# Performance work log

Measured on AMD Instinct MI355X. Metric: run time of the kernel, lower is better.

The kernel has to match this reference:

```python
import jax, jax.numpy as jnp
from jax import lax
import numpy as np

VOCAB, EMB, HID, ENC, ATT, P = 10000, 512, 1024, 2048, 512, 196
B, T = 64, 160
PAD_IDX = 3

def setup_inputs() -> dict:
    key = jax.random.key(0)
    ks = jax.random.split(key, 20)
    s = 0.02
    emb = jax.random.normal(ks[0], (VOCAB, EMB), jnp.float32) * s
    emb = emb.at[PAD_IDX].set(0.0)
    return {
        'image_embedding': jax.random.normal(ks[1], (B, P, ENC), jnp.float32),
        'padded_sentence': jax.random.randint(ks[2], (B, T), 0, VOCAB),
        'enc_h': jax.random.normal(ks[3], (2, B, HID // 2), jnp.float32),
        'enc_c': jax.random.normal(ks[4], (2, B, HID // 2), jnp.float32),
        'sentence_lens': jax.random.randint(ks[5], (B,), 1, T + 1),
        'emb': emb,
        'Wea': jax.random.normal(ks[6], (ATT, ENC), jnp.float32) * s,
        'bea': jnp.zeros((ATT,), jnp.float32),
        'Wda': jax.random.normal(ks[7], (ATT, HID), jnp.float32) * s,
        'bda': jnp.zeros((ATT,), jnp.float32),
        'wfa': jax.random.normal(ks[8], (ATT,), jnp.float32) * s,
        'bfa': jnp.zeros((), jnp.float32),
        'Wfb': jax.random.normal(ks[9], (ENC, HID), jnp.float32) * s,
        'bfb': jnp.zeros((ENC,), jnp.float32),
        'Wih': jax.random.normal(ks[10], (4 * HID, EMB + ENC), jnp.float32) * s,
        'bih': jnp.zeros((4 * HID,), jnp.float32),
        'Whh': jax.random.normal(ks[11], (4 * HID, HID), jnp.float32) * s,
        'bhh': jnp.zeros((4 * HID,), jnp.float32),
    }


def reference(image_embedding, padded_sentence, enc_h, enc_c, sentence_lens,
              emb, Wea, bea, Wda, bda, wfa, bfa, Wfb, bfb, Wih, bih, Whh, bhh):
    Tn = padded_sentence.shape[1]
    # sort by descending length (replicates sentence_lens.sort(descending=True))
    idx = jnp.argsort(-sentence_lens)
    img = image_embedding[idx]                   # [B,P,E]
    sent = padded_sentence[idx]                  # [B,T]
    lens = sentence_lens[idx]                    # [B]
    h0 = jnp.concatenate([enc_h[-2], enc_h[-1]], axis=1)[idx]  # [B,HID]
    c0 = jnp.concatenate([enc_c[-2], enc_c[-1]], axis=1)[idx]
    emb_eff = emb.at[PAD_IDX].set(0.0)           # padding_idx=3
    x_emb = emb_eff[sent]                        # [B,T,EMB]
    # encoder projection is h-independent: hoist out of the scan
    att1 = jnp.einsum('bpe,ae->bpa', img, Wea) + bea  # [B,P,ATT]

    def step(carry, xt):
        h, c = carry
        x_t, t = xt
        active = (t < lens)[:, None]             # ragged mask
        att2 = h @ Wda.T + bda                   # [B,ATT]
        e = jax.nn.relu(att1 + att2[:, None, :]) @ wfa + bfa  # [B,P]
        alpha = jax.nn.softmax(e, axis=1)
        context = jnp.einsum('bp,bpe->be', alpha, img)        # [B,ENC]
        gate = jax.nn.sigmoid(h @ Wfb.T + bfb)
        inp = jnp.concatenate([x_t, gate * context], axis=1)  # [B,EMB+ENC]
        gates = inp @ Wih.T + bih + h @ Whh.T + bhh           # [B,4*HID]
        i, f, g, o = jnp.split(gates, 4, axis=1)
        c_new = jax.nn.sigmoid(f) * c + jax.nn.sigmoid(i) * jnp.tanh(g)
        h_new = jax.nn.sigmoid(o) * jnp.tanh(c_new)
        h = jnp.where(active, h_new, h)
        c = jnp.where(active, c_new, c)
        out_t = jnp.where(active, h_new, 0.0)
        alpha_t = jnp.where(active, alpha, 0.0)
        return (h, c), (out_t, alpha_t)

    (_, _), (outs, alphas) = lax.scan(
        step, (h0, c0), (jnp.swapaxes(x_emb, 0, 1), jnp.arange(Tn)))
    outputs = jnp.swapaxes(outs, 0, 1)           # [B,T,HID]
    alphas = jnp.swapaxes(alphas, 0, 1)          # [B,T,P]
    # replicate the original's final reindex (outputs[ordered_idx], not inverse)
    return outputs[idx], alphas[idx]
```

## Files before the change

kernel.cpp:

```cpp
#include <hip/hip_runtime.h>
#include <hip/hip_bf16.h>
#include <math.h>

#define B 64
#define T 160
#define P 196
#define ENC 2048
#define ATT 512
#define EMB 512
#define HID 1024
#define KTOT 3584
#define N2 2560
#define KT4 112
#define NTHR 1024
#define NBLK 256
#define NGRP 16
#define GRPSZ (NBLK/NGRP)

typedef __attribute__((ext_vector_type(8))) short bf16x8;
typedef __attribute__((ext_vector_type(4))) float f32x4;
typedef float __attribute__((ext_vector_type(4))) vf4;

__device__ __forceinline__ float sigm(float x){ return 1.0f/(1.0f+__expf(-x)); }
__device__ __forceinline__ float bfu(short s){ return __uint_as_float(((unsigned)(unsigned short)s) << 16); }

__device__ __forceinline__ float ldgf(const float* p){ return *(const volatile float*)p; }
__device__ __forceinline__ void stgf(float* p, float v){ *(volatile float*)p = v; }
__device__ __forceinline__ void stgu(unsigned* p, unsigned v){ *(volatile unsigned*)p = v; }
__device__ __forceinline__ unsigned pkbf(float a, float b){
    unsigned ua = (unsigned)__bfloat16_as_ushort(__float2bfloat16(a));
    unsigned ub = (unsigned)__bfloat16_as_ushort(__float2bfloat16(b));
    return ua | (ub << 16);
}

__device__ __forceinline__ void gbar(unsigned* bar, unsigned k){
    asm volatile("s_waitcnt vmcnt(0)" ::: "memory");
    __syncthreads();
    if (threadIdx.x == 0){
        unsigned g = blockIdx.x & (NGRP-1);
        unsigned* gcnt = bar + g*256;
        unsigned* top  = bar + NGRP*256;
        unsigned old = __hip_atomic_fetch_add(gcnt, 1u, __ATOMIC_RELAXED, __HIP_MEMORY_SCOPE_AGENT);
        if (old == (k + 1u)*GRPSZ - 1u){
            __hip_atomic_fetch_add(top, 1u, __ATOMIC_RELAXED, __HIP_MEMORY_SCOPE_AGENT);
        }
        unsigned target = (k + 1u)*NGRP;
        while (*(volatile unsigned*)top < target){
            __builtin_amdgcn_s_sleep(1);
        }
    }
    __syncthreads();
    asm volatile("" ::: "memory");
}

__global__ void k_sort(const int* lens, int* idx, int* rank, unsigned* barCnt, int* nAct){
    __shared__ int L[B];
    int i = threadIdx.x;
    L[i] = lens[i];
    if (i <= NGRP) barCnt[i*256] = 0u;
    __syncthreads();
    int li = L[i];
    int r = 0;
    for (int j = 0; j < B; ++j){
        int lj = L[j];
        if (lj > li || (lj == li && j < i)) r++;
    }
    rank[i] = r;
    idx[r] = i;
    for (int tt = i; tt < T; tt += B){
        int c = 0;
        for (int j = 0; j < B; ++j) c += (L[j] > tt) ? 1 : 0;
        nAct[tt] = c;
    }
}

__global__ void k_init_hc(const float* enc_h, const float* enc_c, const int* idx,
                          float* h, float* c, __hip_bfloat16* hbR0){
    int j = blockIdx.x;
    int o = idx[j];
    for (int k = threadIdx.x; k < HID; k += blockDim.x){
        float hv = (k < 512) ? enc_h[o*512 + k] : enc_h[B*512 + o*512 + (k-512)];
        float cv = (k < 512) ? enc_c[o*512 + k] : enc_c[B*512 + o*512 + (k-512)];
        h[j*HID + k] = hv;
        c[j*HID + k] = cv;
        hbR0[j*HID + k] = __float2bfloat16(hv);
    }
}

__global__ void k_cvt_wcat(const float* Wih, const float* Whh, __hip_bfloat16* Wfrag){
    size_t i = (size_t)blockIdx.x*256 + threadIdx.x;
    int e = (int)(i & 7);
    size_t t2 = i >> 3;
    int lane = (int)(t2 & 63);
    size_t t3 = t2 >> 6;
    int kt = (int)(t3 % KT4);
    int strip = (int)(t3 / KT4);
    int n = strip*16 + (lane & 15);
    int r = (n & 3)*HID + (n >> 2);
    int k = kt*32 + (lane >> 4)*8 + e;
    float v = (k < EMB+ENC) ? Wih[(size_t)r*(EMB+ENC) + k]
                            : Whh[(size_t)r*HID + (k - EMB - ENC)];
    Wfrag[i] = __float2bfloat16(v);
}

__global__ void k_bsum(const float* bih, const float* bhh, float* bsum){
    int n = blockIdx.x*256 + threadIdx.x;
    int r = (n & 3)*HID + (n >> 2);
    bsum[n] = bih[r] + bhh[r];
}

__global__ void k_cvt_w2(const float* Wda, const float* bda, const float* Wfb, const float* bfb,
                         __hip_bfloat16* W2, float* bias2){
    int n = blockIdx.x;
    const float* src = (n < ATT) ? (Wda + (size_t)n*HID) : (Wfb + (size_t)(n-ATT)*HID);
    __hip_bfloat16* dst = W2 + (size_t)n*HID;
    for (int k = threadIdx.x; k < HID; k += 256) dst[k] = __float2bfloat16(src[k]);
    if (threadIdx.x == 0) bias2[n] = (n < ATT) ? bda[n] : bfb[n-ATT];
}

__global__ void k_cvt_emb(const float* emb, __hip_bfloat16* emb_bf){
    size_t i = (size_t)blockIdx.x*256 + threadIdx.x;
    emb_bf[i] = __float2bfloat16(emb[i]);
}

__global__ void k_cvt_wea(const float* Wea, __hip_bfloat16* Wea_bf){
    int n = blockIdx.x;
    for (int k = threadIdx.x; k < ENC; k += 256)
        Wea_bf[(size_t)n*ENC + k] = __float2bfloat16(Wea[(size_t)n*ENC + k]);
}

__global__ void k_cvt_img(const float* img, const int* idx, __hip_bfloat16* img_s){
    int j = blockIdx.y;
    int o = idx[j];
    size_t off = (size_t)blockIdx.x*256 + threadIdx.x;
    img_s[(size_t)j*P*ENC + off] = __float2bfloat16(img[(size_t)o*P*ENC + off]);
}

__global__ __launch_bounds__(256) void k_att1m(const __hip_bfloat16* img_s, const __hip_bfloat16* Wea_bf,
                                               const float* bea, __hip_bfloat16* att1w){
    int m0 = blockIdx.x * 64, n0 = blockIdx.y * 64;
    int tid = threadIdx.x, w = tid >> 6, l = tid & 63, lm = l & 15, lk = l >> 4;
    const short* ap = (const short*)img_s + (size_t)(m0 + 16*w + lm)*ENC + 8*lk;
    const short* bp = (const short*)Wea_bf + (size_t)(n0 + lm)*ENC + 8*lk;
    f32x4 acc[4];
    #pragma unroll
    for (int nt=0; nt<4; ++nt) acc[nt] = (f32x4){0.f,0.f,0.f,0.f};
    #pragma unroll 4
    for (int kt = 0; kt < ENC/32; ++kt){
        bf16x8 a = *(const bf16x8*)(ap + kt*32);
        #pragma unroll
        for (int nt=0; nt<4; ++nt){
            bf16x8 bb = *(const bf16x8*)(bp + (size_t)nt*16*ENC + kt*32);
            acc[nt] = __builtin_amdgcn_mfma_f32_16x16x32_bf16(a, bb, acc[nt], 0,0,0);
        }
    }
    #pragma unroll
    for (int nt=0; nt<4; ++nt){
        int n = n0 + nt*16 + lm;
        float bv = bea[n];
        #pragma unroll
        for (int r=0; r<4; ++r){
            int m = m0 + 16*w + 4*lk + r;
            att1w[(size_t)m*ATT + n] = __float2bfloat16(acc[nt][r] + bv);
        }
    }
}

struct SP {
    const __hip_bfloat16 *att1w, *img_s, *emb_bf, *Wfrag, *W2;
    const float *bsum, *bias2, *wfa, *bfa;
    const int *sent, *idx, *rank, *lens, *nAct;
    float *D2;
    __hip_bfloat16 *gcR, *hbR;
    float *hF0, *hF1, *cW;
    float *outH, *outA;
    unsigned *barCnt;
};

__global__ __launch_bounds__(1024, 4) void k_scan(SP p){
    __shared__ short WcatL[KT4*64*8];
    __shared__ union {
        struct { float Dp[4][64][17]; float hS[64][4]; int tokL[64], lensL[64], wLs[64]; } gem;
        struct { float att2L[512]; float wfaL[512]; float red[1024]; float aL[208]; float ctxP[8][512]; } p23;
    } sh;

    int b = blockIdx.x, tid = threadIdx.x;
    int w = tid >> 6, l = tid & 63, lm = l & 15, lk = l >> 4;
    unsigned bk = 0;

    {
        const bf16x8* src = (const bf16x8*)((const short*)p.Wfrag + (size_t)b*KT4*64*8);
        bf16x8* dst = (bf16x8*)WcatL;
        #pragma unroll
        for (int i = 0; i < KT4*64/NTHR; ++i) dst[tid + i*NTHR] = src[tid + i*NTHR];
    }
    __syncthreads();

    float bfa0 = p.bfa[0];

    for (int t = 0; t < T; ++t){
        const __hip_bfloat16* hbIn = p.hbR + (size_t)t*B*HID;
        __hip_bfloat16*       hbOut = p.hbR + (size_t)(t+1)*B*HID;
        const __hip_bfloat16* gcT  = p.gcR + (size_t)t*B*ENC;
        const float* hFIn = (t & 1) ? p.hF1 : p.hF0;
        float*       hFOut = (t & 1) ? p.hF0 : p.hF1;
        int nAct = p.nAct[t];

        if (b < N2/16){
            int n0 = b*16;
            int rt = w & 3, kq = w >> 2;
            if (16*rt < nAct){
                const short* ap = (const short*)hbIn + (size_t)(16*rt + lm)*HID + kq*256 + 8*lk;
                const short* bp = (const short*)p.W2 + (size_t)(n0 + lm)*HID + kq*256 + 8*lk;
                f32x4 acc = {0.f,0.f,0.f,0.f};
                #pragma unroll
                for (int kt = 0; kt < 8; ++kt){
                    bf16x8 a = *(const bf16x8*)(ap + kt*32);
                    bf16x8 bb = *(const bf16x8*)(bp + kt*32);
                    acc = __builtin_amdgcn_mfma_f32_16x16x32_bf16(a, bb, acc, 0,0,0);
                }
                #pragma unroll
                for (int r=0; r<4; ++r) sh.gem.Dp[kq][16*rt + 4*lk + r][lm] = acc[r];
            }
            __syncthreads();
            int m = tid >> 4, nl = tid & 15;
            if (m < nAct){
                stgf(&p.D2[m*N2 + n0 + nl],
                     sh.gem.Dp[0][m][nl] + sh.gem.Dp[1][m][nl]
                   + sh.gem.Dp[2][m][nl] + sh.gem.Dp[3][m][nl] + p.bias2[n0 + nl]);
            }
        }
        gbar(p.barCnt, bk++);

        {
            int j = b & 63, q = b >> 6;
            int o = p.idx[j], wj = p.rank[j], lj = p.lens[o];
            if (t < lj){
                if (tid < 512){
                    sh.p23.att2L[tid] = ldgf(&p.D2[j*N2 + tid]);
                    sh.p23.wfaL[tid]  = p.wfa[tid];
                }
                __syncthreads();

                int pp = tid & 255, ah = tid >> 8;
                float acc = 0.f;
                if (pp < P){
                    const short* ar = (const short*)p.att1w + (size_t)(j*P + pp)*ATT + ah*128;
                    #pragma unroll 8
                    for (int k8 = 0; k8 < 16; ++k8){
                        bf16x8 v = *(const bf16x8*)(ar + k8*8);
                        #pragma unroll
                        for (int z=0; z<8; ++z){
                            int a = ah*128 + k8*8 + z;
                            acc += fmaxf(bfu(v[z]) + sh.p23.att2L[a], 0.f) * sh.p23.wfaL[a];
                        }
                    }
                }
                sh.p23.red[tid] = acc;
                __syncthreads();
                float e = -1e30f;
                if (tid < P) e = sh.p23.red[tid] + sh.p23.red[tid+256] + sh.p23.red[tid+512] + sh.p23.red[tid+768] + bfa0;
                __syncthreads();
                sh.p23.red[tid] = (tid < P) ? e : -1e30f;
                __syncthreads();
                for (int s = 512; s > 0; s >>= 1){
                    if (tid < s) sh.p23.red[tid] = fmaxf(sh.p23.red[tid], sh.p23.red[tid+s]);
                    __syncthreads();
                }
                float m = sh.p23.red[0];
                __syncthreads();
                float ex = (tid < P) ? __expf(e - m) : 0.f;
                sh.p23.red[tid] = ex;
                __syncthreads();
                for (int s = 512; s > 0; s >>= 1){
                    if (tid < s) sh.p23.red[tid] += sh.p23.red[tid+s];
                    __syncthreads();
                }
                float ssum = sh.p23.red[0];
                if (tid < P){
                    float alpha = ex / ssum;
                    sh.p23.aL[tid] = alpha;
                    if (q == 0) p.outA[((size_t)(wj*T + t))*P + tid] = alpha;
                }
                if (tid >= P && tid < 208) sh.p23.aL[tid] = 0.f;
                __syncthreads();

                const short* ib = (const short*)p.img_s + (size_t)j*P*ENC + q*512 + l*8;
                float a8[8];
                #pragma unroll
                for (int z=0; z<8; ++z) a8[z] = 0.f;
                #pragma unroll 4
                for (int i = 0; i < 13; ++i){
                    int pp2 = w + 16*i;
                    int pr = (pp2 < P) ? pp2 : 0;
                    bf16x8 v = *(const bf16x8*)(ib + (size_t)pr*ENC);
                    float al = sh.p23.aL[pp2];
                    #pragma unroll
                    for (int z=0; z<8; ++z) a8[z] += al * bfu(v[z]);
                }
                if (w < 8){
                    #pragma unroll
                    for (int z=0; z<8; ++z) sh.p23.ctxP[w][l*8+z] = a8[z];
                }
                __syncthreads();
                if (w >= 8){
                    #pragma unroll
                    for (int z=0; z<8; ++z) sh.p23.ctxP[w-8][l*8+z] += a8[z];
                }
                __syncthreads();
                if (tid < 256){
                    int d0 = 2*tid;
                    float c0 = 0.f, c1 = 0.f;
                    #pragma unroll
                    for (int r=0; r<8; ++r){ c0 += sh.p23.ctxP[r][d0]; c1 += sh.p23.ctxP[r][d0+1]; }
                    int eg0 = q*512 + d0;
                    float g0 = sigm(ldgf(&p.D2[j*N2 + ATT + eg0]));
                    float g1 = sigm(ldgf(&p.D2[j*N2 + ATT + eg0 + 1]));
                    stgu((unsigned*)((short*)gcT + j*ENC + eg0), pkbf(g0*c0, g1*c1));
                }
            } else {
                if (q == 0 && tid < P) p.outA[((size_t)(wj*T + t))*P + tid] = 0.f;
            }
        }
        gbar(p.barCnt, bk++);

        {
            if (tid < 64){
                int o = p.idx[tid];
                sh.gem.tokL[tid] = p.sent[o*T + t];
                sh.gem.lensL[tid] = p.lens[o];
                sh.gem.wLs[tid] = p.rank[tid];
            }
            __syncthreads();
            int rt = w & 3, kq = w >> 2;
            if (16*rt < nAct){
                int mrow = 16*rt + lm;
                int tok = sh.gem.tokL[mrow];
                const short* aEmb = (const short*)p.emb_bf + (size_t)tok*EMB + 8*lk;
                const short* aGc  = (const short*)gcT + (size_t)mrow*ENC + 8*lk;
                const short* aH   = (const short*)hbIn + (size_t)mrow*HID + 8*lk;
                const bf16x8* BL = (const bf16x8*)WcatL;
                f32x4 acc = {0.f,0.f,0.f,0.f};
                if (kq == 0){
                    #pragma unroll 8
                    for (int kt = 0; kt < 16; ++kt){
                        bf16x8 a = *(const bf16x8*)(aEmb + kt*32);
                        acc = __builtin_amdgcn_mfma_f32_16x16x32_bf16(a, BL[kt*64 + l], acc, 0,0,0);
                    }
                    #pragma unroll 6
                    for (int kt = 16; kt < 28; ++kt){
                        bf16x8 a = *(const bf16x8*)(aGc + (kt-16)*32);
                        acc = __builtin_amdgcn_mfma_f32_16x16x32_bf16(a, BL[kt*64 + l], acc, 0,0,0);
                    }
                } else if (kq == 1){
                    #pragma unroll 7
                    for (int kt = 28; kt < 56; ++kt){
                        bf16x8 a = *(const bf16x8*)(aGc + (kt-16)*32);
                        acc = __builtin_amdgcn_mfma_f32_16x16x32_bf16(a, BL[kt*64 + l], acc, 0,0,0);
                    }
                } else if (kq == 2){
                    #pragma unroll 6
                    for (int kt = 56; kt < 80; ++kt){
                        bf16x8 a = *(const bf16x8*)(aGc + (kt-16)*32);
                        acc = __builtin_amdgcn_mfma_f32_16x16x32_bf16(a, BL[kt*64 + l], acc, 0,0,0);
                    }
                    #pragma unroll
                    for (int kt = 80; kt < 84; ++kt){
                        bf16x8 a = *(const bf16x8*)(aH + (kt-80)*32);
                        acc = __builtin_amdgcn_mfma_f32_16x16x32_bf16(a, BL[kt*64 + l], acc, 0,0,0);
                    }
                } else {
                    #pragma unroll 7
                    for (int kt = 84; kt < 112; ++kt){
                        bf16x8 a = *(const bf16x8*)(aH + (kt-80)*32);
                        acc = __builtin_amdgcn_mfma_f32_16x16x32_bf16(a, BL[kt*64 + l], acc, 0,0,0);
                    }
                }
                #pragma unroll
                for (int r=0; r<4; ++r) sh.gem.Dp[kq][16*rt + 4*lk + r][lm] = acc[r];
            }
            __syncthreads();
            if (tid < 256){
                int j2 = tid & 63, du = tid >> 6;
                int u = 4*b + du;
                float g4[4];
                #pragma unroll
                for (int g=0; g<4; ++g){
                    int nl = 4*du + g;
                    g4[g] = sh.gem.Dp[0][j2][nl] + sh.gem.Dp[1][j2][nl]
                          + sh.gem.Dp[2][j2][nl] + sh.gem.Dp[3][j2][nl] + p.bsum[16*b + nl];
                }
                float ig = sigm(g4[0]), fg = sigm(g4[1]), gg = tanhf(g4[2]), og = sigm(g4[3]);
                float cOld = p.cW[j2*HID + u];
                float cNew = fg*cOld + ig*gg;
                float hNew = og*tanhf(cNew);
                bool active = (t < sh.gem.lensL[j2]);
                float hOld = hFIn[j2*HID + u];
                float hKeep = active ? hNew : hOld;
                hFOut[j2*HID + u] = hKeep;
                sh.gem.hS[j2][du] = hKeep;
                p.cW[j2*HID + u] = active ? cNew : cOld;
                p.outH[((size_t)sh.gem.wLs[j2]*T + t)*HID + u] = active ? hNew : 0.f;
            }
            __syncthreads();
            if (tid < 128){
                int j2 = tid & 63, dp = tid >> 6;
                int u0 = 4*b + 2*dp;
                stgu((unsigned*)((short*)hbOut + j2*HID + u0),
                     pkbf(sh.gem.hS[j2][2*dp], sh.gem.hS[j2][2*dp+1]));
            }
        }
        gbar(p.barCnt, bk++);
    }
}

extern "C" void kernel_launch(void* const* d_in, const int* in_sizes, int n_in,
                              void* d_out, int out_size, void* d_ws, size_t ws_size,
                              hipStream_t stream) {
    const float* img   = (const float*)d_in[0];
    const int*   sent  = (const int*)  d_in[1];
    const float* enc_h = (const float*)d_in[2];
    const float* enc_c = (const float*)d_in[3];
    const int*   lens  = (const int*)  d_in[4];
    const float* emb   = (const float*)d_in[5];
    const float* Wea   = (const float*)d_in[6];
    const float* bea   = (const float*)d_in[7];
    const float* Wda   = (const float*)d_in[8];
    const float* bda   = (const float*)d_in[9];
    const float* wfa   = (const float*)d_in[10];
    const float* bfa   = (const float*)d_in[11];
    const float* Wfb   = (const float*)d_in[12];
    const float* bfb   = (const float*)d_in[13];
    const float* Wih   = (const float*)d_in[14];
    const float* bih   = (const float*)d_in[15];
    const float* Whh   = (const float*)d_in[16];
    const float* bhh   = (const float*)d_in[17];

    float* outH = (float*)d_out;
    float* outA = outH + (size_t)B*T*HID;

    char* wsb = (char*)d_ws;
    size_t off = 0;
    int* idxW  = (int*)(wsb + off); off += 256;
    int* rankW = (int*)(wsb + off); off += 256;
    int* nActW = (int*)(wsb + off); off += 1024;
    unsigned* barCnt = (unsigned*)(wsb + off); off += 32768;
    __hip_bfloat16* att1w = (__hip_bfloat16*)(wsb + off); off += (size_t)B*P*ATT*2;
    __hip_bfloat16* img_s = (__hip_bfloat16*)(wsb + off); off += (size_t)B*P*ENC*2;
    __hip_bfloat16* emb_bf= (__hip_bfloat16*)(wsb + off); off += (size_t)10000*EMB*2;
    __hip_bfloat16* Wfrag = (__hip_bfloat16*)(wsb + off); off += (size_t)4*HID*KTOT*2;
    __hip_bfloat16* W2    = (__hip_bfloat16*)(wsb + off); off += (size_t)N2*HID*2;
    __hip_bfloat16* Wea_bf= (__hip_bfloat16*)(wsb + off); off += (size_t)ATT*ENC*2;
    float* bsum  = (float*)(wsb + off); off += 4*HID*4;
    float* bias2 = (float*)(wsb + off); off += N2*4;
    float* hA    = (float*)(wsb + off); off += B*HID*4;
    float* hB    = (float*)(wsb + off); off += B*HID*4;
    float* cWs   = (float*)(wsb + off); off += B*HID*4;
    float* D2    = (float*)(wsb + off); off += (size_t)B*N2*4;
    __hip_bfloat16* gcR = (__hip_bfloat16*)(wsb + off); off += (size_t)T*B*ENC*2;
    __hip_bfloat16* hbR = (__hip_bfloat16*)(wsb + off); off += (size_t)(T+1)*B*HID*2;

    k_sort<<<1, 64, 0, stream>>>(lens, idxW, rankW, barCnt, nActW);
    k_init_hc<<<B, 256, 0, stream>>>(enc_h, enc_c, idxW, hA, cWs, hbR);
    k_cvt_wcat<<<57344, 256, 0, stream>>>(Wih, Whh, Wfrag);
    k_bsum<<<16, 256, 0, stream>>>(bih, bhh, bsum);
    k_cvt_w2<<<N2, 256, 0, stream>>>(Wda, bda, Wfb, bfb, W2, bias2);
    k_cvt_emb<<<20000, 256, 0, stream>>>(emb, emb_bf);
    k_cvt_wea<<<ATT, 256, 0, stream>>>(Wea, Wea_bf);
    k_cvt_img<<<dim3(P*ENC/256, B), 256, 0, stream>>>(img, idxW, img_s);
    k_att1m<<<dim3((B*P)/64, ATT/64), 256, 0, stream>>>(img_s, Wea_bf, bea, att1w);

    SP sp;
    sp.att1w = att1w; sp.img_s = img_s; sp.emb_bf = emb_bf; sp.Wfrag = Wfrag; sp.W2 = W2;
    sp.bsum = bsum; sp.bias2 = bias2; sp.wfa = wfa; sp.bfa = bfa;
    sp.sent = sent; sp.idx = idxW; sp.rank = rankW; sp.lens = lens; sp.nAct = nActW;
    sp.D2 = D2; sp.gcR = gcR; sp.hbR = hbR;
    sp.hF0 = hA; sp.hF1 = hB; sp.cW = cWs;
    sp.outH = outH; sp.outA = outA;
    sp.barCnt = barCnt;

    void* args[] = { &sp };
    hipLaunchCooperativeKernel(reinterpret_cast<void*>(k_scan), dim3(NBLK), dim3(NTHR),
                               args, 0, stream);
}
```

Baseline: 7.452 ms.

## Split grid barrier into arrive/wait with hierarchical release and overlap work

```diff
diff --git a/kernel.cpp b/kernel.cpp
--- a/kernel.cpp
+++ b/kernel.cpp
@@ -33,31 +33,42 @@
     return ua | (ub << 16);
 }
 
-__device__ __forceinline__ void gbar(unsigned* bar, unsigned k){
+__device__ __forceinline__ void gbar_arrive(unsigned* bar, unsigned k){
     asm volatile("s_waitcnt vmcnt(0)" ::: "memory");
     __syncthreads();
     if (threadIdx.x == 0){
         unsigned g = blockIdx.x & (NGRP-1);
-        unsigned* gcnt = bar + g*256;
-        unsigned* top  = bar + NGRP*256;
-        unsigned old = __hip_atomic_fetch_add(gcnt, 1u, __ATOMIC_RELAXED, __HIP_MEMORY_SCOPE_AGENT);
+        unsigned old = __hip_atomic_fetch_add(bar + g*256, 1u, __ATOMIC_RELAXED, __HIP_MEMORY_SCOPE_AGENT);
         if (old == (k + 1u)*GRPSZ - 1u){
-            __hip_atomic_fetch_add(top, 1u, __ATOMIC_RELAXED, __HIP_MEMORY_SCOPE_AGENT);
-        }
-        unsigned target = (k + 1u)*NGRP;
-        while (*(volatile unsigned*)top < target){
-            __builtin_amdgcn_s_sleep(1);
+            __hip_atomic_fetch_add(bar + NGRP*256, 1u, __ATOMIC_RELAXED, __HIP_MEMORY_SCOPE_AGENT);
+        }
+    }
+}
+__device__ __forceinline__ void gbar_wait(unsigned* bar, unsigned k){
+    if (threadIdx.x == 0){
+        unsigned b = blockIdx.x;
+        if (b < NGRP){
+            volatile unsigned* top = bar + NGRP*256;
+            while (*top < (k + 1u)*NGRP) __builtin_amdgcn_s_sleep(2);
+            *(volatile unsigned*)(bar + (NGRP + 1 + b)*256) = k + 1u;
+        } else {
+            volatile unsigned* rel = bar + (NGRP + 1 + (b & (NGRP-1)))*256;
+            while (*rel < k + 1u) __builtin_amdgcn_s_sleep(2);
         }
     }
     __syncthreads();
     asm volatile("" ::: "memory");
+}
+__device__ __forceinline__ void gbar(unsigned* bar, unsigned k){
+    gbar_arrive(bar, k);
+    gbar_wait(bar, k);
 }
 
 __global__ void k_sort(const int* lens, int* idx, int* rank, unsigned* barCnt, int* nAct){
     __shared__ int L[B];
     int i = threadIdx.x;
     L[i] = lens[i];
-    if (i <= NGRP) barCnt[i*256] = 0u;
+    if (i < 33) barCnt[i*256] = 0u;
     __syncthreads();
     int li = L[i];
     int r = 0;
@@ -230,14 +241,14 @@
                    + sh.gem.Dp[2][m][nl] + sh.gem.Dp[3][m][nl] + p.bias2[n0 + nl]);
             }
         }
-        gbar(p.barCnt, bk++);
-
+        gbar(p.barCnt, bk); bk++;
+
+        int jj = b & 63, qq = b >> 6;
+        int oo = p.idx[jj], wjj = p.rank[jj], ljj = p.lens[oo];
         {
-            int j = b & 63, q = b >> 6;
-            int o = p.idx[j], wj = p.rank[j], lj = p.lens[o];
-            if (t < lj){
+            if (t < ljj){
                 if (tid < 512){
-                    sh.p23.att2L[tid] = ldgf(&p.D2[j*N2 + tid]);
+                    sh.p23.att2L[tid] = ldgf(&p.D2[jj*N2 + tid]);
                     sh.p23.wfaL[tid]  = p.wfa[tid];
                 }
                 __syncthreads();
@@ -245,7 +256,7 @@
                 int pp = tid & 255, ah = tid >> 8;
                 float acc = 0.f;
                 if (pp < P){
-                    const short* ar = (const short*)p.att1w + (size_t)(j*P + pp)*ATT + ah*128;
+                    const short* ar = (const short*)p.att1w + (size_t)(jj*P + pp)*ATT + ah*128;
                     #pragma unroll 8
                     for (int k8 = 0; k8 < 16; ++k8){
                         bf16x8 v = *(const bf16x8*)(ar + k8*8);
@@ -277,15 +288,11 @@
                     __syncthreads();
                 }
                 float ssum = sh.p23.red[0];
-                if (tid < P){
-                    float alpha = ex / ssum;
-                    sh.p23.aL[tid] = alpha;
-                    if (q == 0) p.outA[((size_t)(wj*T + t))*P + tid] = alpha;
-                }
+                if (tid < P) sh.p23.aL[tid] = ex / ssum;
                 if (tid >= P && tid < 208) sh.p23.aL[tid] = 0.f;
                 __syncthreads();
 
-                const short* ib = (const short*)p.img_s + (size_t)j*P*ENC + q*512 + l*8;
+                const short* ib = (const short*)p.img_s + (size_t)jj*P*ENC + qq*512 + l*8;
                 float a8[8];
                 #pragma unroll
                 for (int z=0; z<8; ++z) a8[z] = 0.f;
@@ -313,40 +320,64 @@
                     float c0 = 0.f, c1 = 0.f;
                     #pragma unroll
                     for (int r=0; r<8; ++r){ c0 += sh.p23.ctxP[r][d0]; c1 += sh.p23.ctxP[r][d0+1]; }
-                    int eg0 = q*512 + d0;
-                    float g0 = sigm(ldgf(&p.D2[j*N2 + ATT + eg0]));
-                    float g1 = sigm(ldgf(&p.D2[j*N2 + ATT + eg0 + 1]));
-                    stgu((unsigned*)((short*)gcT + j*ENC + eg0), pkbf(g0*c0, g1*c1));
-                }
-            } else {
-                if (q == 0 && tid < P) p.outA[((size_t)(wj*T + t))*P + tid] = 0.f;
+                    int eg0 = qq*512 + d0;
+                    float g0 = sigm(ldgf(&p.D2[jj*N2 + ATT + eg0]));
+                    float g1 = sigm(ldgf(&p.D2[jj*N2 + ATT + eg0 + 1]));
+                    stgu((unsigned*)((short*)gcT + jj*ENC + eg0), pkbf(g0*c0, g1*c1));
+                }
             }
         }
-        gbar(p.barCnt, bk++);
-
+        gbar_arrive(p.barCnt, bk);
+
+        if (qq == 0 && tid < P){
+            float av = (t < ljj) ? sh.p23.aL[tid] : 0.f;
+            p.outA[((size_t)(wjj*T + t))*P + tid] = av;
+        }
+        __syncthreads();
+
+        if (tid < 64){
+            int o = p.idx[tid];
+            sh.gem.tokL[tid] = p.sent[o*T + t];
+            sh.gem.lensL[tid] = p.lens[o];
+            sh.gem.wLs[tid] = p.rank[tid];
+        }
+        __syncthreads();
         {
-            if (tid < 64){
-                int o = p.idx[tid];
-                sh.gem.tokL[tid] = p.sent[o*T + t];
-                sh.gem.lensL[tid] = p.lens[o];
-                sh.gem.wLs[tid] = p.rank[tid];
-            }
-            __syncthreads();
             int rt = w & 3, kq = w >> 2;
-            if (16*rt < nAct){
-                int mrow = 16*rt + lm;
+            bool act = (16*rt < nAct);
+            int mrow = 16*rt + lm;
+            f32x4 acc = {0.f,0.f,0.f,0.f};
+            const short* aEmb = 0; const short* aGc = 0; const short* aH = 0;
+            const bf16x8* BL = (const bf16x8*)WcatL;
+            if (act){
                 int tok = sh.gem.tokL[mrow];
-                const short* aEmb = (const short*)p.emb_bf + (size_t)tok*EMB + 8*lk;
-                const short* aGc  = (const short*)gcT + (size_t)mrow*ENC + 8*lk;
-                const short* aH   = (const short*)hbIn + (size_t)mrow*HID + 8*lk;
-                const bf16x8* BL = (const bf16x8*)WcatL;
-                f32x4 acc = {0.f,0.f,0.f,0.f};
+                aEmb = (const short*)p.emb_bf + (size_t)tok*EMB + 8*lk;
+                aGc  = (const short*)gcT + (size_t)mrow*ENC + 8*lk;
+                aH   = (const short*)hbIn + (size_t)mrow*HID + 8*lk;
                 if (kq == 0){
                     #pragma unroll 8
                     for (int kt = 0; kt < 16; ++kt){
                         bf16x8 a = *(const bf16x8*)(aEmb + kt*32);
                         acc = __builtin_amdgcn_mfma_f32_16x16x32_bf16(a, BL[kt*64 + l], acc, 0,0,0);
                     }
+                } else if (kq == 2){
+                    #pragma unroll
+                    for (int kt = 80; kt < 84; ++kt){
+                        bf16x8 a = *(const bf16x8*)(aH + (kt-80)*32);
+                        acc = __builtin_amdgcn_mfma_f32_16x16x32_bf16(a, BL[kt*64 + l], acc, 0,0,0);
+                    }
+                } else if (kq == 3){
+                    #pragma unroll 7
+                    for (int kt = 84; kt < 112; ++kt){
+                        bf16x8 a = *(const bf16x8*)(aH + (kt-80)*32);
+                        acc = __builtin_amdgcn_mfma_f32_16x16x32_bf16(a, BL[kt*64 + l], acc, 0,0,0);
+                    }
+                }
+            }
+            gbar_wait(p.barCnt, bk); bk++;
+
+            if (act){
+                if (kq == 0){
                     #pragma unroll 6
                     for (int kt = 16; kt < 28; ++kt){
                         bf16x8 a = *(const bf16x8*)(aGc + (kt-16)*32);
@@ -364,53 +395,48 @@
                         bf16x8 a = *(const bf16x8*)(aGc + (kt-16)*32);
                         acc = __builtin_amdgcn_mfma_f32_16x16x32_bf16(a, BL[kt*64 + l], acc, 0,0,0);
                     }
-                    #pragma unroll
-                    for (int kt = 80; kt < 84; ++kt){
-                        bf16x8 a = *(const bf16x8*)(aH + (kt-80)*32);
-                        acc = __builtin_amdgcn_mfma_f32_16x16x32_bf16(a, BL[kt*64 + l], acc, 0,0,0);
-                    }
-                } else {
-                    #pragma unroll 7
-                    for (int kt = 84; kt < 112; ++kt){
-                        bf16x8 a = *(const bf16x8*)(aH + (kt-80)*32);
-                        acc = __builtin_amdgcn_mfma_f32_16x16x32_bf16(a, BL[kt*64 + l], acc, 0,0,0);
-                    }
                 }
                 #pragma unroll
                 for (int r=0; r<4; ++r) sh.gem.Dp[kq][16*rt + 4*lk + r][lm] = acc[r];
             }
-            __syncthreads();
-            if (tid < 256){
-                int j2 = tid & 63, du = tid >> 6;
-                int u = 4*b + du;
-                float g4[4];
-                #pragma unroll
-                for (int g=0; g<4; ++g){
-                    int nl = 4*du + g;
-                    g4[g] = sh.gem.Dp[0][j2][nl] + sh.gem.Dp[1][j2][nl]
-                          + sh.gem.Dp[2][j2][nl] + sh.gem.Dp[3][j2][nl] + p.bsum[16*b + nl];
-                }
-                float ig = sigm(g4[0]), fg = sigm(g4[1]), gg = tanhf(g4[2]), og = sigm(g4[3]);
-                float cOld = p.cW[j2*HID + u];
-                float cNew = fg*cOld + ig*gg;
-                float hNew = og*tanhf(cNew);
-                bool active = (t < sh.gem.lensL[j2]);
-                float hOld = hFIn[j2*HID + u];
-                float hKeep = active ? hNew : hOld;
-                hFOut[j2*HID + u] = hKeep;
-                sh.gem.hS[j2][du] = hKeep;
-                p.cW[j2*HID + u] = active ? cNew : cOld;
-                p.outH[((size_t)sh.gem.wLs[j2]*T + t)*HID + u] = active ? hNew : 0.f;
+        }
+        __syncthreads();
+
+        int j2 = tid & 63, du = tid >> 6;
+        int u = 4*b + du;
+        float cNew = 0.f, hNew = 0.f, hKeep = 0.f, cOld = 0.f;
+        bool active = false;
+        if (tid < 256){
+            float g4[4];
+            #pragma unroll
+            for (int g=0; g<4; ++g){
+                int nl = 4*du + g;
+                g4[g] = sh.gem.Dp[0][j2][nl] + sh.gem.Dp[1][j2][nl]
+                      + sh.gem.Dp[2][j2][nl] + sh.gem.Dp[3][j2][nl] + p.bsum[16*b + nl];
             }
-            __syncthreads();
-            if (tid < 128){
-                int j2 = tid & 63, dp = tid >> 6;
-                int u0 = 4*b + 2*dp;
-                stgu((unsigned*)((short*)hbOut + j2*HID + u0),
-                     pkbf(sh.gem.hS[j2][2*dp], sh.gem.hS[j2][2*dp+1]));
-            }
-        }
-        gbar(p.barCnt, bk++);
+            float ig = sigm(g4[0]), fg = sigm(g4[1]), gg = tanhf(g4[2]), og = sigm(g4[3]);
+            cOld = p.cW[j2*HID + u];
+            cNew = fg*cOld + ig*gg;
+            hNew = og*tanhf(cNew);
+            active = (t < sh.gem.lensL[j2]);
+            float hOld = hFIn[j2*HID + u];
+            hKeep = active ? hNew : hOld;
+            sh.gem.hS[j2][du] = hKeep;
+        }
+        __syncthreads();
+        if (tid < 128){
+            int jb = tid & 63, dp = tid >> 6;
+            int u0 = 4*b + 2*dp;
+            stgu((unsigned*)((short*)hbOut + jb*HID + u0),
+                 pkbf(sh.gem.hS[jb][2*dp], sh.gem.hS[jb][2*dp+1]));
+        }
+        gbar_arrive(p.barCnt, bk);
+        if (tid < 256){
+            p.cW[j2*HID + u] = active ? cNew : cOld;
+            hFOut[j2*HID + u] = hKeep;
+            p.outH[((size_t)sh.gem.wLs[j2]*T + t)*HID + u] = active ? hNew : 0.f;
+        }
+        gbar_wait(p.barCnt, bk); bk++;
     }
 }
 
@@ -444,7 +470,7 @@
     int* idxW  = (int*)(wsb + off); off += 256;
     int* rankW = (int*)(wsb + off); off += 256;
     int* nActW = (int*)(wsb + off); off += 1024;
-    unsigned* barCnt = (unsigned*)(wsb + off); off += 32768;
+    unsigned* barCnt = (unsigned*)(wsb + off); off += 36864;
     __hip_bfloat16* att1w = (__hip_bfloat16*)(wsb + off); off += (size_t)B*P*ATT*2;
     __hip_bfloat16* img_s = (__hip_bfloat16*)(wsb + off); off += (size_t)B*P*ENC*2;
     __hip_bfloat16* emb_bf= (__hip_bfloat16*)(wsb + off); off += (size_t)10000*EMB*2;
```

Measured after the change: 7.031 ms. 5.6% less time.
